# Kernel tuning notes

Hardware: AMD Instinct MI355X
Metric: run time of the kernel (lower is better)

Reference implementation:

```python
import jax, jax.numpy as jnp
import numpy as np

N_NODES = 10000
LN_EPS = 1e-5


def _gcn(x, W, b, src, dst):
    # GraphConvolution: linear transform then sum-aggregate messages over edges.
    sup = x @ W                               # [B, N, H]
    msg = sup[:, src, :]                      # [B, E, H] gather from source nodes
    agg = jax.vmap(lambda m: jax.ops.segment_sum(m, dst, num_segments=N_NODES))(msg)
    return agg + b


def _layernorm(x, g, b):
    mu = jnp.mean(x, axis=-1, keepdims=True)
    var = jnp.var(x, axis=-1, keepdims=True)
    return (x - mu) * jax.lax.rsqrt(var + LN_EPS) * g + b


def _attention_pool(x, W, u, num_iterations=3):
    # x: [B, N, d] -> r: [B, 1, d]
    a = jnp.tanh(x @ W) @ u                   # [B, N]
    alpha = jax.nn.softmax(a, axis=1)
    r = jnp.einsum('bn,bnd->bd', alpha, x)
    for _ in range(num_iterations):
        beta = jax.nn.softmax(jnp.einsum('bnd,bd->bn', x, r), axis=1)
        r = jnp.einsum('bn,bnd->bd', beta, x)
    return r[:, None, :]


def _forward(x, src, dst, W_conv0, b_conv0, W_convs, b_convs,
             mW1, mb1, mW2, mb2, mW3, mb3,
             ln1_g, ln1_b, ln2_g, ln2_b, attnW, attnu, fW1, fb1, fW2, fb2,
             fcW, fcb):
    gelu = lambda t: jax.nn.gelu(t, approximate=False)
    # stacked GCN layers (first layer distinct input dim)
    x = gelu(_gcn(x, W_conv0, b_conv0, src, dst))
    for i in range(W_convs.shape[0]):
        x = gelu(_gcn(x, W_convs[i], b_convs[i], src, dst))
    # dropout is identity in eval mode
    # MLP head
    x = jax.nn.relu(x @ mW1 + mb1)
    x = jax.nn.relu(x @ mW2 + mb2)
    x = x @ mW3 + mb3
    # Encoder: 2 layers of (attention-pool residual + LN + FFN residual + LN)
    for i in range(2):
        x = x + _attention_pool(x, attnW[i], attnu[i])   # broadcast [B,1,d]
        x = _layernorm(x, ln1_g[i], ln1_b[i])
        h = jax.nn.relu(x @ fW1[i] + fb1[i]) @ fW2[i] + fb2[i]
        x = _layernorm(x + h, ln2_g[i], ln2_b[i])
    x = x @ fcW + fcb                          # [B, N, out]
    return x.mean(axis=1)                      # [B, out]


def setup_inputs() -> dict:
    key = jax.random.key(0)
    ks = jax.random.split(key, 32)
    B, N, E = 4, N_NODES, 160000
    F_in, H, D, A, OUT = 128, 256, 256, 8, 10
    s = lambda k, *shape: jax.random.normal(k, shape, jnp.float32) * 0.05
    return {
        'x': jax.random.normal(ks[0], (B, N, F_in), jnp.float32),
        'src': jax.random.randint(ks[1], (E,), 0, N, jnp.int32),
        'dst': jax.random.randint(ks[2], (E,), 0, N, jnp.int32),
        'W_conv0': s(ks[3], F_in, H), 'b_conv0': s(ks[4], H),
        'W_convs': s(ks[5], 3, H, H), 'b_convs': s(ks[6], 3, H),
        'mW1': s(ks[7], H, H // 2), 'mb1': s(ks[8], H // 2),
        'mW2': s(ks[9], H // 2, H // 4), 'mb2': s(ks[10], H // 4),
        'mW3': s(ks[11], H // 4, D), 'mb3': s(ks[12], D),
        'ln1_g': jnp.ones((2, D), jnp.float32), 'ln1_b': jnp.zeros((2, D), jnp.float32),
        'ln2_g': jnp.ones((2, D), jnp.float32), 'ln2_b': jnp.zeros((2, D), jnp.float32),
        'attnW': s(ks[13], 2, D, A), 'attnu': s(ks[14], 2, A),
        'fW1': s(ks[15], 2, D, H), 'fb1': s(ks[16], 2, H),
        'fW2': s(ks[17], 2, H, D), 'fb2': s(ks[18], 2, D),
        'fcW': s(ks[19], D, OUT), 'fcb': s(ks[20], OUT),
    }


def reference(x, src, dst, W_conv0, b_conv0, W_convs, b_convs,
              mW1, mb1, mW2, mb2, mW3, mb3,
              ln1_g, ln1_b, ln2_g, ln2_b, attnW, attnu, fW1, fb1, fW2, fb2,
              fcW, fcb):
    return _forward(x, src, dst, W_conv0, b_conv0, W_convs, b_convs,
                    mW1, mb1, mW2, mb2, mW3, mb3,
                    ln1_g, ln1_b, ln2_g, ln2_b, attnW, attnu, fW1, fb1, fW2, fb2,
                    fcW, fcb)
```

## Files before the change

kernel.cpp:

```cpp
#include <hip/hip_runtime.h>
#include <math.h>

#define NN 10000
#define NB 4
#define NE 160000
#define DM 256
#define MR (NB * NN)
#define LN_EPS 1e-5f
#define PCH 40
#define NCH (NN / PCH)
#define CCH 100

typedef __attribute__((ext_vector_type(8))) short short8;
typedef __attribute__((ext_vector_type(4))) float floatx4;


__device__ inline float bf2f(unsigned short u) {
    unsigned int x = ((unsigned int)u) << 16;
    float f;
    __builtin_memcpy(&f, &x, 4);
    return f;
}

__device__ inline unsigned short f2bf(float f) {
    unsigned int x;
    __builtin_memcpy(&x, &f, 4);
    unsigned int r = x + 0x7FFFu + ((x >> 16) & 1u);
    return (unsigned short)(r >> 16);
}

__device__ inline float gelu_exact(float x) {
    return 0.5f * x * (1.0f + erff(x * 0.70710678118654752f));
}

__device__ inline float waveAllReduce(float v) {
#pragma unroll
    for (int off = 32; off > 0; off >>= 1) v += __shfl_xor(v, off, 64);
    return v;
}

__device__ inline void gld16(const unsigned short* g, unsigned short* l) {
    __builtin_amdgcn_global_load_lds((const __attribute__((address_space(1))) void*)g,
                                     (__attribute__((address_space(3))) void*)l, 16, 0, 0);
}


__global__ void zero_i32_kernel(int* p, int n) {
    int i = blockIdx.x * 256 + threadIdx.x;
    if (i < n) p[i] = 0;
}

__global__ void cvt_bf16_kernel(const float* __restrict__ in, unsigned short* __restrict__ out, int n) {
    int i = blockIdx.x * 256 + threadIdx.x;
    if (i < n) out[i] = f2bf(in[i]);
}

struct TD { const float* src; unsigned short* dst; int K; int N; };
struct TDs { TD d[11]; };

__global__ void transpose_all_kernel(TDs tds) {
    TD t = tds.d[blockIdx.y];
    int idx = blockIdx.x * 256 + threadIdx.x;
    int total = t.K * t.N;
    if (idx < total) {
        int n = idx / t.K;
        int k = idx - n * t.K;
        t.dst[idx] = f2bf(t.src[(size_t)k * t.N + n]);
    }
}


__global__ void hist_kernel(const int* __restrict__ dst, int* __restrict__ counts, int e) {
    int i = blockIdx.x * 256 + threadIdx.x;
    if (i < e) atomicAdd(&counts[dst[i]], 1);
}

__global__ __launch_bounds__(256) void scan_kernel(const int* __restrict__ counts,
                                                   int* __restrict__ row_ptr,
                                                   int* __restrict__ fill_pos, int n) {
    __shared__ int sums[256];
    int tid = threadIdx.x;
    int chunk = (n + 255) / 256;
    int s0 = tid * chunk;
    int s1 = min(n, s0 + chunk);
    int local = 0;
    for (int i = s0; i < s1; i++) local += counts[i];
    sums[tid] = local;
    __syncthreads();
    for (int off = 1; off < 256; off <<= 1) {
        int v = (tid >= off) ? sums[tid - off] : 0;
        __syncthreads();
        sums[tid] += v;
        __syncthreads();
    }
    int base = (tid == 0) ? 0 : sums[tid - 1];
    for (int i = s0; i < s1; i++) {
        row_ptr[i] = base;
        fill_pos[i] = base;
        base += counts[i];
    }
    if (tid == 255) row_ptr[n] = sums[255];
}

__global__ void fill_kernel(const int* __restrict__ src, const int* __restrict__ dst,
                            int* __restrict__ fill_pos, int* __restrict__ csr_src, int e) {
    int i = blockIdx.x * 256 + threadIdx.x;
    if (i < e) {
        int p = atomicAdd(&fill_pos[dst[i]], 1);
        csr_src[p] = src[i];
    }
}


template <int BN, int CM>
__global__ __launch_bounds__(256) void mfma_gemm_kernel(
    const unsigned short* __restrict__ A, const unsigned short* __restrict__ Bt,
    const float* __restrict__ bias, void* __restrict__ Cp, int K, int N, int act) {
    constexpr int NBF = BN / 32;
    __shared__ unsigned short AsL[4 * 64 * 8];
    __shared__ unsigned short BsL[(BN / 16) * 64 * 8];

    const int tid = threadIdx.x;
    const int w = tid >> 6, l = tid & 63;
    const int wm = w >> 1, wn = w & 1;
    const int bm0 = blockIdx.y * 64;
    const int bn0 = blockIdx.x * BN;
    const int lm = l & 15, lq = l >> 4;

    floatx4 acc[2][NBF];
#pragma unroll
    for (int mi = 0; mi < 2; mi++)
#pragma unroll
        for (int ni = 0; ni < NBF; ni++) acc[mi][ni] = (floatx4){0.f, 0.f, 0.f, 0.f};

    const int s_ll = tid & 63;
    const int a_row = bm0 + (tid >> 6) * 16 + (s_ll & 15);
    const int s_kc = (s_ll >> 4) * 8;

    for (int k0 = 0; k0 < K; k0 += 32) {
        gld16(&A[(size_t)a_row * K + k0 + s_kc], &AsL[tid * 8]);
#pragma unroll
        for (int cc = 0; cc < BN / 64; cc++) {
            int c = tid + cc * 256;
            int rown = bn0 + (c >> 6) * 16 + (c & 15);
            int kc = k0 + ((c & 63) >> 4) * 8;
            gld16(&Bt[(size_t)rown * K + kc], &BsL[c * 8]);
        }
        __syncthreads();
        short8 af[2], bfv[NBF];
#pragma unroll
        for (int mi = 0; mi < 2; mi++) af[mi] = *(short8*)&AsL[((wm * 2 + mi) * 64 + l) * 8];
#pragma unroll
        for (int ni = 0; ni < NBF; ni++) bfv[ni] = *(short8*)&BsL[((wn * NBF + ni) * 64 + l) * 8];
#pragma unroll
        for (int mi = 0; mi < 2; mi++)
#pragma unroll
            for (int ni = 0; ni < NBF; ni++)
                acc[mi][ni] = __builtin_amdgcn_mfma_f32_16x16x32_bf16(af[mi], bfv[ni], acc[mi][ni], 0, 0, 0);
        __syncthreads();
    }

#pragma unroll
    for (int ni = 0; ni < NBF; ni++) {
        int col = bn0 + (wn * NBF + ni) * 16 + lm;
        float bv = bias ? bias[col] : 0.0f;
#pragma unroll
        for (int mi = 0; mi < 2; mi++) {
            int row0 = bm0 + (wm * 2 + mi) * 16 + lq * 4;
#pragma unroll
            for (int r = 0; r < 4; r++) {
                int row = row0 + r;
                float v = acc[mi][ni][r] + bv;
                if (act == 1) v = fmaxf(v, 0.0f);
                if (CM == 0) {
                    ((float*)Cp)[(size_t)row * N + col] = v;
                } else if (CM == 1) {
                    ((unsigned short*)Cp)[(size_t)row * N + col] = f2bf(v);
                } else {
                    int bb = row / NN;
                    int nn = row - bb * NN;
                    ((unsigned short*)Cp)[(size_t)nn * (NB * DM) + bb * DM + col] = f2bf(v);
                }
            }
        }
    }
}


__global__ __launch_bounds__(256) void agg_kernel(const unsigned short* __restrict__ sup,
                                                  const int* __restrict__ row_ptr,
                                                  const int* __restrict__ csr_src,
                                                  const float* __restrict__ bias,
                                                  unsigned short* __restrict__ out) {
    int n = blockIdx.x;
    int w = threadIdx.x >> 6, l = threadIdx.x & 63;
    int s = row_ptr[n], e = row_ptr[n + 1];
    const int off = w * DM + l * 4;
    float a0 = 0.f, a1 = 0.f, a2 = 0.f, a3 = 0.f;
    int j = s;
    for (; j + 8 <= e; j += 8) {
        int idx[8];
#pragma unroll
        for (int k = 0; k < 8; k++) idx[k] = csr_src[j + k];
        ushort4 v[8];
#pragma unroll
        for (int k = 0; k < 8; k++) v[k] = *(const ushort4*)&sup[(size_t)idx[k] * (NB * DM) + off];
#pragma unroll
        for (int k = 0; k < 8; k++) {
            a0 += bf2f(v[k].x); a1 += bf2f(v[k].y);
            a2 += bf2f(v[k].z); a3 += bf2f(v[k].w);
        }
    }
    for (; j < e; j++) {
        ushort4 v = *(const ushort4*)&sup[(size_t)csr_src[j] * (NB * DM) + off];
        a0 += bf2f(v.x); a1 += bf2f(v.y); a2 += bf2f(v.z); a3 += bf2f(v.w);
    }
    int d0 = l * 4;
    const float4 bv = *(const float4*)&bias[d0];
    ushort4 o;
    o.x = f2bf(gelu_exact(a0 + bv.x));
    o.y = f2bf(gelu_exact(a1 + bv.y));
    o.z = f2bf(gelu_exact(a2 + bv.z));
    o.w = f2bf(gelu_exact(a3 + bv.w));
    *(ushort4*)&out[((size_t)w * NN + n) * DM + d0] = o;
}


template <int MODE>
__global__ __launch_bounds__(256) void attn_pool_kernel(const unsigned short* __restrict__ x16,
                                                        const float* __restrict__ W,
                                                        const float* __restrict__ u,
                                                        const float* __restrict__ r_in,
                                                        float* __restrict__ pm,
                                                        float* __restrict__ pl,
                                                        float* __restrict__ pv) {
    int c = blockIdx.x, b = blockIdx.y;
    int tid = threadIdx.x, w = tid >> 6, l = tid & 63;
    float4 rv = {0, 0, 0, 0};
    float u0[8];
    if (MODE == 1) {
        rv = *(const float4*)&r_in[b * DM + l * 4];
    } else {
#pragma unroll
        for (int j = 0; j < 8; j++) u0[j] = u[j];
    }
    int n0 = c * PCH;
    float m = -INFINITY, L = 0.0f;
    float v0 = 0.f, v1 = 0.f, v2 = 0.f, v3 = 0.f;
    for (int n = n0 + w; n < n0 + PCH; n += 4) {
        ushort4 xb = *(const ushort4*)&x16[((size_t)b * NN + n) * DM + l * 4];
        float x0 = bf2f(xb.x), x1 = bf2f(xb.y), x2 = bf2f(xb.z), x3 = bf2f(xb.w);
        float s;
        if (MODE == 1) {
            s = x0 * rv.x + x1 * rv.y + x2 * rv.z + x3 * rv.w;
            s = waveAllReduce(s);
        } else {
            const float4* Wv = (const float4*)W;
            int d0 = l * 4;
            float xs[4] = {x0, x1, x2, x3};
            float t[8] = {0, 0, 0, 0, 0, 0, 0, 0};
#pragma unroll
            for (int dd = 0; dd < 4; dd++) {
                float4 w0 = Wv[(d0 + dd) * 2 + 0];
                float4 w1 = Wv[(d0 + dd) * 2 + 1];
                t[0] += xs[dd] * w0.x; t[1] += xs[dd] * w0.y; t[2] += xs[dd] * w0.z; t[3] += xs[dd] * w0.w;
                t[4] += xs[dd] * w1.x; t[5] += xs[dd] * w1.y; t[6] += xs[dd] * w1.z; t[7] += xs[dd] * w1.w;
            }
#pragma unroll
            for (int jj = 0; jj < 8; jj++) t[jj] = waveAllReduce(t[jj]);
            s = 0.f;
#pragma unroll
            for (int jj = 0; jj < 8; jj++) s += tanhf(t[jj]) * u0[jj];
        }
        if (s > m) {
            float sc = __expf(m - s);
            L *= sc; v0 *= sc; v1 *= sc; v2 *= sc; v3 *= sc;
            m = s;
        }
        float wgt = __expf(s - m);
        L += wgt;
        v0 += wgt * x0; v1 += wgt * x1; v2 += wgt * x2; v3 += wgt * x3;
    }
    __shared__ float sm[4], sl[4];
    __shared__ float sv[4][DM];
    if (l == 0) { sm[w] = m; sl[w] = L; }
    float4 vv = {v0, v1, v2, v3};
    *(float4*)&sv[w][l * 4] = vv;
    __syncthreads();
    int d = tid;
    float M = fmaxf(fmaxf(sm[0], sm[1]), fmaxf(sm[2], sm[3]));
    float e0 = __expf(sm[0] - M), e1 = __expf(sm[1] - M);
    float e2 = __expf(sm[2] - M), e3 = __expf(sm[3] - M);
    float Lt = e0 * sl[0] + e1 * sl[1] + e2 * sl[2] + e3 * sl[3];
    float vd = e0 * sv[0][d] + e1 * sv[1][d] + e2 * sv[2][d] + e3 * sv[3][d];
    pv[((size_t)b * NCH + c) * DM + d] = vd;
    if (d == 0) {
        pm[b * NCH + c] = M;
        pl[b * NCH + c] = Lt;
    }
}

__global__ __launch_bounds__(256) void attn_combine_kernel(const float* __restrict__ pm,
                                                           const float* __restrict__ pl,
                                                           const float* __restrict__ pv,
                                                           float* __restrict__ r) {
    int b = blockIdx.x, tid = threadIdx.x;
    __shared__ float red[256];
    __shared__ float se[NCH];
    float mv = -INFINITY;
    for (int c = tid; c < NCH; c += 256) mv = fmaxf(mv, pm[b * NCH + c]);
    red[tid] = mv;
    __syncthreads();
    for (int off = 128; off > 0; off >>= 1) {
        if (tid < off) red[tid] = fmaxf(red[tid], red[tid + off]);
        __syncthreads();
    }
    float M = red[0];
    __syncthreads();
    float lsum = 0.0f;
    for (int c = tid; c < NCH; c += 256) {
        float e = __expf(pm[b * NCH + c] - M);
        se[c] = e;
        lsum += e * pl[b * NCH + c];
    }
    red[tid] = lsum;
    __syncthreads();
    for (int off = 128; off > 0; off >>= 1) {
        if (tid < off) red[tid] += red[tid + off];
        __syncthreads();
    }
    float L = red[0];
    __syncthreads();
    float acc = 0.0f;
    for (int c = 0; c < NCH; c++) acc += se[c] * pv[((size_t)b * NCH + c) * DM + tid];
    r[b * DM + tid] = acc / L;
}


__global__ __launch_bounds__(256) void ln_bcast_kernel(const unsigned short* __restrict__ x16,
                                                       const float* __restrict__ r,
                                                       const float* __restrict__ g,
                                                       const float* __restrict__ bt,
                                                       unsigned short* __restrict__ out16) {
    int l = threadIdx.x & 63, w = threadIdx.x >> 6;
    int row = blockIdx.x * 4 + w;
    int b = row / NN;
    ushort4 xb = *(const ushort4*)&x16[(size_t)row * DM + l * 4];
    float4 rv = *(const float4*)(r + (size_t)b * DM + l * 4);
    float4 y;
    y.x = bf2f(xb.x) + rv.x; y.y = bf2f(xb.y) + rv.y;
    y.z = bf2f(xb.z) + rv.z; y.w = bf2f(xb.w) + rv.w;
    float s = y.x + y.y + y.z + y.w;
    float sq = y.x * y.x + y.y * y.y + y.z * y.z + y.w * y.w;
    s = waveAllReduce(s);
    sq = waveAllReduce(sq);
    float mean = s * (1.0f / 256.0f);
    float var = sq * (1.0f / 256.0f) - mean * mean;
    float rstd = rsqrtf(var + LN_EPS);
    float4 gv = *(const float4*)(g + l * 4);
    float4 bv = *(const float4*)(bt + l * 4);
    ushort4 o;
    o.x = f2bf((y.x - mean) * rstd * gv.x + bv.x);
    o.y = f2bf((y.y - mean) * rstd * gv.y + bv.y);
    o.z = f2bf((y.z - mean) * rstd * gv.z + bv.z);
    o.w = f2bf((y.w - mean) * rstd * gv.w + bv.w);
    *(ushort4*)&out16[(size_t)row * DM + l * 4] = o;
}

__global__ __launch_bounds__(256) void ln_elem_kernel(const unsigned short* __restrict__ x16,
                                                      const float* __restrict__ h,
                                                      const float* __restrict__ g,
                                                      const float* __restrict__ bt,
                                                      unsigned short* __restrict__ out16) {
    int l = threadIdx.x & 63, w = threadIdx.x >> 6;
    int row = blockIdx.x * 4 + w;
    ushort4 xb = *(const ushort4*)&x16[(size_t)row * DM + l * 4];
    float4 hv = *(const float4*)(h + (size_t)row * DM + l * 4);
    float4 y;
    y.x = bf2f(xb.x) + hv.x; y.y = bf2f(xb.y) + hv.y;
    y.z = bf2f(xb.z) + hv.z; y.w = bf2f(xb.w) + hv.w;
    float s = y.x + y.y + y.z + y.w;
    float sq = y.x * y.x + y.y * y.y + y.z * y.z + y.w * y.w;
    s = waveAllReduce(s);
    sq = waveAllReduce(sq);
    float mean = s * (1.0f / 256.0f);
    float var = sq * (1.0f / 256.0f) - mean * mean;
    float rstd = rsqrtf(var + LN_EPS);
    float4 gv = *(const float4*)(g + l * 4);
    float4 bv = *(const float4*)(bt + l * 4);
    ushort4 o;
    o.x = f2bf((y.x - mean) * rstd * gv.x + bv.x);
    o.y = f2bf((y.y - mean) * rstd * gv.y + bv.y);
    o.z = f2bf((y.z - mean) * rstd * gv.z + bv.z);
    o.w = f2bf((y.w - mean) * rstd * gv.w + bv.w);
    *(ushort4*)&out16[(size_t)row * DM + l * 4] = o;
}


__global__ __launch_bounds__(256) void colsum_kernel(const unsigned short* __restrict__ x16,
                                                     float* __restrict__ pcol) {
    int b = blockIdx.y, c = blockIdx.x, d = threadIdx.x;
    int n0 = c * CCH, n1 = n0 + CCH;
    float acc = 0.0f;
    for (int n = n0; n < n1; n++) acc += bf2f(x16[((size_t)b * NN + n) * DM + d]);
    pcol[((size_t)b * (NN / CCH) + c) * DM + d] = acc;
}

__global__ __launch_bounds__(256) void final_kernel(const float* __restrict__ pcol,
                                                    const float* __restrict__ fcW,
                                                    const float* __restrict__ fcb,
                                                    float* __restrict__ out) {
    int b = blockIdx.x, d = threadIdx.x;
    __shared__ float sx[DM];
    float acc = 0.0f;
    for (int c = 0; c < NN / CCH; c++) acc += pcol[((size_t)b * (NN / CCH) + c) * DM + d];
    sx[d] = acc;
    __syncthreads();
    if (d < 10) {
        float o = 0.0f;
        for (int k = 0; k < DM; k++) o += sx[k] * fcW[k * 10 + d];
        out[b * 10 + d] = o * (1.0f / NN) + fcb[d];
    }
}


extern "C" void kernel_launch(void* const* d_in, const int* in_sizes, int n_in,
                              void* d_out, int out_size, void* d_ws, size_t ws_size,
                              hipStream_t stream) {
    const float* x_in    = (const float*)d_in[0];
    const int*   src     = (const int*)d_in[1];
    const int*   dst     = (const int*)d_in[2];
    const float* W_conv0 = (const float*)d_in[3];
    const float* b_conv0 = (const float*)d_in[4];
    const float* W_convs = (const float*)d_in[5];
    const float* b_convs = (const float*)d_in[6];
    const float* mW1 = (const float*)d_in[7];
    const float* mb1 = (const float*)d_in[8];
    const float* mW2 = (const float*)d_in[9];
    const float* mb2 = (const float*)d_in[10];
    const float* mW3 = (const float*)d_in[11];
    const float* mb3 = (const float*)d_in[12];
    const float* ln1_g = (const float*)d_in[13];
    const float* ln1_b = (const float*)d_in[14];
    const float* ln2_g = (const float*)d_in[15];
    const float* ln2_b = (const float*)d_in[16];
    const float* attnW = (const float*)d_in[17];
    const float* attnu = (const float*)d_in[18];
    const float* fW1 = (const float*)d_in[19];
    const float* fb1 = (const float*)d_in[20];
    const float* fW2 = (const float*)d_in[21];
    const float* fb2 = (const float*)d_in[22];
    const float* fcW = (const float*)d_in[23];
    const float* fcb = (const float*)d_in[24];
    float* out = (float*)d_out;

    char* p = (char*)d_ws;
    auto alloc = [&](size_t bytes) { char* q = p; p += (bytes + 255) & ~(size_t)255; return q; };
    float* A = (float*)alloc((size_t)MR * DM * 4);
    unsigned short* sup16 = (unsigned short*)alloc((size_t)MR * DM * 2);
    unsigned short* act16 = (unsigned short*)alloc((size_t)MR * DM * 2);
    unsigned short* b16   = (unsigned short*)alloc((size_t)MR * DM * 2);
    unsigned short* t1    = (unsigned short*)alloc((size_t)MR * 128 * 2);
    unsigned short* t2    = (unsigned short*)alloc((size_t)MR * 64 * 2);
    unsigned short* wt    = (unsigned short*)alloc((size_t)548864 * 2);
    float* rbuf = (float*)alloc(NB * DM * 4);
    float* pm0  = (float*)alloc(NB * NCH * 4);
    float* pl0  = (float*)alloc(NB * NCH * 4);
    float* pv0  = (float*)alloc((size_t)NB * NCH * DM * 4);
    float* pcol = (float*)alloc((size_t)NB * (NN / CCH) * DM * 4);
    int* counts   = (int*)alloc(NN * 4);
    int* row_ptr  = (int*)alloc((NN + 1) * 4);
    int* fill_pos = (int*)alloc(NN * 4);
    int* csr_src  = (int*)alloc(NE * 4);

    unsigned short* Wt_conv0 = wt;
    unsigned short* Wt_convs = Wt_conv0 + 32768;
    unsigned short* mW1t = Wt_convs + 196608;
    unsigned short* mW2t = mW1t + 32768;
    unsigned short* mW3t = mW2t + 8192;
    unsigned short* fW1t = mW3t + 16384;
    unsigned short* fW2t = fW1t + 131072;

    const dim3 blk(256);

    zero_i32_kernel<<<(NN + 255) / 256, blk, 0, stream>>>(counts, NN);
    hist_kernel<<<(NE + 255) / 256, blk, 0, stream>>>(dst, counts, NE);
    scan_kernel<<<1, blk, 0, stream>>>(counts, row_ptr, fill_pos, NN);
    fill_kernel<<<(NE + 255) / 256, blk, 0, stream>>>(src, dst, fill_pos, csr_src, NE);

    TDs tds;
    tds.d[0]  = {W_conv0, Wt_conv0, 128, 256};
    tds.d[1]  = {W_convs + 0 * 65536, Wt_convs + 0 * 65536, 256, 256};
    tds.d[2]  = {W_convs + 1 * 65536, Wt_convs + 1 * 65536, 256, 256};
    tds.d[3]  = {W_convs + 2 * 65536, Wt_convs + 2 * 65536, 256, 256};
    tds.d[4]  = {mW1, mW1t, 256, 128};
    tds.d[5]  = {mW2, mW2t, 128, 64};
    tds.d[6]  = {mW3, mW3t, 64, 256};
    tds.d[7]  = {fW1 + 0 * 65536, fW1t + 0 * 65536, 256, 256};
    tds.d[8]  = {fW1 + 1 * 65536, fW1t + 1 * 65536, 256, 256};
    tds.d[9]  = {fW2 + 0 * 65536, fW2t + 0 * 65536, 256, 256};
    tds.d[10] = {fW2 + 1 * 65536, fW2t + 1 * 65536, 256, 256};
    transpose_all_kernel<<<dim3(256, 11), blk, 0, stream>>>(tds);

    cvt_bf16_kernel<<<(MR * 128 + 255) / 256, blk, 0, stream>>>(x_in, t1, MR * 128);

    mfma_gemm_kernel<128, 2><<<dim3(2, MR / 64), blk, 0, stream>>>(t1, Wt_conv0, nullptr, sup16, 128, 256, 0);
    agg_kernel<<<NN, blk, 0, stream>>>(sup16, row_ptr, csr_src, b_conv0, act16);
    for (int i = 0; i < 3; i++) {
        mfma_gemm_kernel<128, 2><<<dim3(2, MR / 64), blk, 0, stream>>>(act16, Wt_convs + (size_t)i * 65536, nullptr, sup16, 256, 256, 0);
        agg_kernel<<<NN, blk, 0, stream>>>(sup16, row_ptr, csr_src, b_convs + (size_t)i * 256, act16);
    }

    mfma_gemm_kernel<128, 1><<<dim3(1, MR / 64), blk, 0, stream>>>(act16, mW1t, mb1, t1, 256, 128, 1);
    mfma_gemm_kernel<64, 1><<<dim3(1, MR / 64), blk, 0, stream>>>(t1, mW2t, mb2, t2, 128, 64, 1);
    mfma_gemm_kernel<128, 1><<<dim3(2, MR / 64), blk, 0, stream>>>(t2, mW3t, mb3, act16, 64, 256, 0);

    const dim3 poolGrid(NCH, NB);
    for (int i = 0; i < 2; i++) {
        const float* Wp = attnW + (size_t)i * DM * 8;
        const float* up = attnu + (size_t)i * 8;
        attn_pool_kernel<0><<<poolGrid, blk, 0, stream>>>(act16, Wp, up, nullptr, pm0, pl0, pv0);
        attn_combine_kernel<<<NB, blk, 0, stream>>>(pm0, pl0, pv0, rbuf);
        for (int it = 0; it < 3; it++) {
            attn_pool_kernel<1><<<poolGrid, blk, 0, stream>>>(act16, nullptr, nullptr, rbuf, pm0, pl0, pv0);
            attn_combine_kernel<<<NB, blk, 0, stream>>>(pm0, pl0, pv0, rbuf);
        }
        ln_bcast_kernel<<<MR / 4, blk, 0, stream>>>(act16, rbuf, ln1_g + (size_t)i * DM,
                                                    ln1_b + (size_t)i * DM, b16);
        mfma_gemm_kernel<128, 1><<<dim3(2, MR / 64), blk, 0, stream>>>(b16, fW1t + (size_t)i * 65536,
                                                                       fb1 + (size_t)i * DM, sup16, 256, 256, 1);
        mfma_gemm_kernel<128, 0><<<dim3(2, MR / 64), blk, 0, stream>>>(sup16, fW2t + (size_t)i * 65536,
                                                                       fb2 + (size_t)i * DM, A, 256, 256, 0);
        ln_elem_kernel<<<MR / 4, blk, 0, stream>>>(b16, A, ln2_g + (size_t)i * DM,
                                                   ln2_b + (size_t)i * DM, act16);
    }

    colsum_kernel<<<dim3(NN / CCH, NB), blk, 0, stream>>>(act16, pcol);
    final_kernel<<<NB, blk, 0, stream>>>(pcol, fcW, fcb, out);
}
```

Before: 790.9 us.

## Double-buffer MFMA GEMM loads and fuse FFN second GEMM with residual LayerNorm

Makes K a template parameter and double-buffers the LDS tiles, so the next K-slice is loaded while MFMAs run on the current one and one barrier per iteration goes away. Adds a gemm_ln_kernel that computes the full 256-wide FFN output row block, adds bias and residual, reduces row statistics across the two wave columns through shared memory, and writes the normalized bf16 output directly. This removes the fp32 intermediate buffer and the separate ln_elem pass, at the cost of a larger per-block tile, more registers and fewer blocks for that GEMM.

After: 770.8 us. 1.03x faster.

```diff
diff --git a/kernel.cpp b/kernel.cpp
--- a/kernel.cpp
+++ b/kernel.cpp
@@ -36,6 +36,12 @@
 __device__ inline float waveAllReduce(float v) {
 #pragma unroll
     for (int off = 32; off > 0; off >>= 1) v += __shfl_xor(v, off, 64);
+    return v;
+}
+
+__device__ inline float group16Reduce(float v) {
+#pragma unroll
+    for (int off = 8; off > 0; off >>= 1) v += __shfl_xor(v, off, 64);
     return v;
 }
 
@@ -112,13 +118,14 @@
 }
 
 
-template <int BN, int CM>
+template <int BN, int CM, int K>
 __global__ __launch_bounds__(256) void mfma_gemm_kernel(
     const unsigned short* __restrict__ A, const unsigned short* __restrict__ Bt,
-    const float* __restrict__ bias, void* __restrict__ Cp, int K, int N, int act) {
+    const float* __restrict__ bias, void* __restrict__ Cp, int N, int act) {
     constexpr int NBF = BN / 32;
-    __shared__ unsigned short AsL[4 * 64 * 8];
-    __shared__ unsigned short BsL[(BN / 16) * 64 * 8];
+    constexpr int NI = K / 32;
+    __shared__ unsigned short AsL[2][4 * 64 * 8];
+    __shared__ unsigned short BsL[2][(BN / 16) * 64 * 8];
 
     const int tid = threadIdx.x;
     const int w = tid >> 6, l = tid & 63;
@@ -133,31 +140,46 @@
 #pragma unroll
         for (int ni = 0; ni < NBF; ni++) acc[mi][ni] = (floatx4){0.f, 0.f, 0.f, 0.f};
 
-    const int s_ll = tid & 63;
-    const int a_row = bm0 + (tid >> 6) * 16 + (s_ll & 15);
-    const int s_kc = (s_ll >> 4) * 8;
-
-    for (int k0 = 0; k0 < K; k0 += 32) {
-        gld16(&A[(size_t)a_row * K + k0 + s_kc], &AsL[tid * 8]);
-#pragma unroll
-        for (int cc = 0; cc < BN / 64; cc++) {
-            int c = tid + cc * 256;
-            int rown = bn0 + (c >> 6) * 16 + (c & 15);
-            int kc = k0 + ((c & 63) >> 4) * 8;
-            gld16(&Bt[(size_t)rown * K + kc], &BsL[c * 8]);
-        }
+    const int a_row = bm0 + (tid >> 6) * 16 + (l & 15);
+    const int s_kc = (l >> 4) * 8;
+    int b_rown[BN / 64], b_kc[BN / 64];
+#pragma unroll
+    for (int cc = 0; cc < BN / 64; cc++) {
+        int c = tid + cc * 256;
+        b_rown[cc] = bn0 + (c >> 6) * 16 + (c & 15);
+        b_kc[cc] = ((c & 63) >> 4) * 8;
+    }
+
+    gld16(&A[(size_t)a_row * K + s_kc], &AsL[0][tid * 8]);
+#pragma unroll
+    for (int cc = 0; cc < BN / 64; cc++) {
+        int c = tid + cc * 256;
+        gld16(&Bt[(size_t)b_rown[cc] * K + b_kc[cc]], &BsL[0][c * 8]);
+    }
+
+#pragma unroll
+    for (int i = 0; i < NI; i++) {
+        const int buf = i & 1;
         __syncthreads();
+        if (i + 1 < NI) {
+            int k0 = (i + 1) * 32;
+            gld16(&A[(size_t)a_row * K + k0 + s_kc], &AsL[buf ^ 1][tid * 8]);
+#pragma unroll
+            for (int cc = 0; cc < BN / 64; cc++) {
+                int c = tid + cc * 256;
+                gld16(&Bt[(size_t)b_rown[cc] * K + k0 + b_kc[cc]], &BsL[buf ^ 1][c * 8]);
+            }
+        }
         short8 af[2], bfv[NBF];
 #pragma unroll
-        for (int mi = 0; mi < 2; mi++) af[mi] = *(short8*)&AsL[((wm * 2 + mi) * 64 + l) * 8];
-#pragma unroll
-        for (int ni = 0; ni < NBF; ni++) bfv[ni] = *(short8*)&BsL[((wn * NBF + ni) * 64 + l) * 8];
+        for (int mi = 0; mi < 2; mi++) af[mi] = *(short8*)&AsL[buf][((wm * 2 + mi) * 64 + l) * 8];
+#pragma unroll
+        for (int ni = 0; ni < NBF; ni++) bfv[ni] = *(short8*)&BsL[buf][((wn * NBF + ni) * 64 + l) * 8];
 #pragma unroll
         for (int mi = 0; mi < 2; mi++)
 #pragma unroll
             for (int ni = 0; ni < NBF; ni++)
                 acc[mi][ni] = __builtin_amdgcn_mfma_f32_16x16x32_bf16(af[mi], bfv[ni], acc[mi][ni], 0, 0, 0);
-        __syncthreads();
     }
 
 #pragma unroll
@@ -181,6 +203,136 @@
                     int nn = row - bb * NN;
                     ((unsigned short*)Cp)[(size_t)nn * (NB * DM) + bb * DM + col] = f2bf(v);
                 }
+            }
+        }
+    }
+}
+
+
+__global__ __launch_bounds__(256) void gemm_ln_kernel(
+    const unsigned short* __restrict__ A,
+    const unsigned short* __restrict__ Bt,
+    const float* __restrict__ bias,
+    const unsigned short* __restrict__ x1,
+    const float* __restrict__ g, const float* __restrict__ bt,
+    unsigned short* __restrict__ out16) {
+    constexpr int K = 256, NBF = 8, NI = K / 32;
+    __shared__ unsigned short AsL[2][4 * 64 * 8];
+    __shared__ unsigned short BsL[2][16 * 64 * 8];
+    __shared__ float rs[2][64], rq[2][64];
+
+    const int tid = threadIdx.x;
+    const int w = tid >> 6, l = tid & 63;
+    const int wm = w >> 1, wn = w & 1;
+    const int bm0 = blockIdx.x * 64;
+    const int lm = l & 15, lq = l >> 4;
+
+    floatx4 acc[2][NBF];
+#pragma unroll
+    for (int mi = 0; mi < 2; mi++)
+#pragma unroll
+        for (int ni = 0; ni < NBF; ni++) acc[mi][ni] = (floatx4){0.f, 0.f, 0.f, 0.f};
+
+    const int a_row = bm0 + (tid >> 6) * 16 + (l & 15);
+    const int s_kc = (l >> 4) * 8;
+    int b_rown[4], b_kc[4];
+#pragma unroll
+    for (int cc = 0; cc < 4; cc++) {
+        int c = tid + cc * 256;
+        b_rown[cc] = (c >> 6) * 16 + (c & 15);
+        b_kc[cc] = ((c & 63) >> 4) * 8;
+    }
+
+    gld16(&A[(size_t)a_row * K + s_kc], &AsL[0][tid * 8]);
+#pragma unroll
+    for (int cc = 0; cc < 4; cc++) {
+        int c = tid + cc * 256;
+        gld16(&Bt[(size_t)b_rown[cc] * K + b_kc[cc]], &BsL[0][c * 8]);
+    }
+
+#pragma unroll
+    for (int i = 0; i < NI; i++) {
+        const int buf = i & 1;
+        __syncthreads();
+        if (i + 1 < NI) {
+            int k0 = (i + 1) * 32;
+            gld16(&A[(size_t)a_row * K + k0 + s_kc], &AsL[buf ^ 1][tid * 8]);
+#pragma unroll
+            for (int cc = 0; cc < 4; cc++) {
+                int c = tid + cc * 256;
+                gld16(&Bt[(size_t)b_rown[cc] * K + k0 + b_kc[cc]], &BsL[buf ^ 1][c * 8]);
+            }
+        }
+        short8 af[2], bfv[NBF];
+#pragma unroll
+        for (int mi = 0; mi < 2; mi++) af[mi] = *(short8*)&AsL[buf][((wm * 2 + mi) * 64 + l) * 8];
+#pragma unroll
+        for (int ni = 0; ni < NBF; ni++) bfv[ni] = *(short8*)&BsL[buf][((wn * NBF + ni) * 64 + l) * 8];
+#pragma unroll
+        for (int mi = 0; mi < 2; mi++)
+#pragma unroll
+            for (int ni = 0; ni < NBF; ni++)
+                acc[mi][ni] = __builtin_amdgcn_mfma_f32_16x16x32_bf16(af[mi], bfv[ni], acc[mi][ni], 0, 0, 0);
+    }
+
+    float fb[NBF], gv[NBF], bv[NBF];
+#pragma unroll
+    for (int ni = 0; ni < NBF; ni++) {
+        int col = (wn * NBF + ni) * 16 + lm;
+        fb[ni] = bias[col];
+        gv[ni] = g[col];
+        bv[ni] = bt[col];
+    }
+    float psum[2][4], psq[2][4];
+#pragma unroll
+    for (int mi = 0; mi < 2; mi++)
+#pragma unroll
+        for (int r = 0; r < 4; r++) { psum[mi][r] = 0.f; psq[mi][r] = 0.f; }
+
+#pragma unroll
+    for (int mi = 0; mi < 2; mi++) {
+        int row0 = bm0 + (wm * 2 + mi) * 16 + lq * 4;
+#pragma unroll
+        for (int r = 0; r < 4; r++) {
+#pragma unroll
+            for (int ni = 0; ni < NBF; ni++) {
+                int col = (wn * NBF + ni) * 16 + lm;
+                float y = bf2f(x1[(size_t)(row0 + r) * DM + col]) + acc[mi][ni][r] + fb[ni];
+                acc[mi][ni][r] = y;
+                psum[mi][r] += y;
+                psq[mi][r] += y * y;
+            }
+        }
+    }
+#pragma unroll
+    for (int mi = 0; mi < 2; mi++)
+#pragma unroll
+        for (int r = 0; r < 4; r++) {
+            float s = group16Reduce(psum[mi][r]);
+            float q = group16Reduce(psq[mi][r]);
+            if (lm == 0) {
+                int rl = (wm * 2 + mi) * 16 + lq * 4 + r;
+                rs[wn][rl] = s;
+                rq[wn][rl] = q;
+            }
+        }
+    __syncthreads();
+#pragma unroll
+    for (int mi = 0; mi < 2; mi++) {
+        int row0 = bm0 + (wm * 2 + mi) * 16 + lq * 4;
+#pragma unroll
+        for (int r = 0; r < 4; r++) {
+            int rl = (wm * 2 + mi) * 16 + lq * 4 + r;
+            float s = rs[0][rl] + rs[1][rl];
+            float q = rq[0][rl] + rq[1][rl];
+            float mean = s * (1.0f / 256.0f);
+            float var = q * (1.0f / 256.0f) - mean * mean;
+            float rstd = rsqrtf(var + LN_EPS);
+#pragma unroll
+            for (int ni = 0; ni < NBF; ni++) {
+                int col = (wn * NBF + ni) * 16 + lm;
+                out16[(size_t)(row0 + r) * DM + col] =
+                    f2bf((acc[mi][ni][r] - mean) * rstd * gv[ni] + bv[ni]);
             }
         }
     }
@@ -350,35 +502,6 @@
     float4 y;
     y.x = bf2f(xb.x) + rv.x; y.y = bf2f(xb.y) + rv.y;
     y.z = bf2f(xb.z) + rv.z; y.w = bf2f(xb.w) + rv.w;
-    float s = y.x + y.y + y.z + y.w;
-    float sq = y.x * y.x + y.y * y.y + y.z * y.z + y.w * y.w;
-    s = waveAllReduce(s);
-    sq = waveAllReduce(sq);
-    float mean = s * (1.0f / 256.0f);
-    float var = sq * (1.0f / 256.0f) - mean * mean;
-    float rstd = rsqrtf(var + LN_EPS);
-    float4 gv = *(const float4*)(g + l * 4);
-    float4 bv = *(const float4*)(bt + l * 4);
-    ushort4 o;
-    o.x = f2bf((y.x - mean) * rstd * gv.x + bv.x);
-    o.y = f2bf((y.y - mean) * rstd * gv.y + bv.y);
-    o.z = f2bf((y.z - mean) * rstd * gv.z + bv.z);
-    o.w = f2bf((y.w - mean) * rstd * gv.w + bv.w);
-    *(ushort4*)&out16[(size_t)row * DM + l * 4] = o;
-}
-
-__global__ __launch_bounds__(256) void ln_elem_kernel(const unsigned short* __restrict__ x16,
-                                                      const float* __restrict__ h,
-                                                      const float* __restrict__ g,
-                                                      const float* __restrict__ bt,
-                                                      unsigned short* __restrict__ out16) {
-    int l = threadIdx.x & 63, w = threadIdx.x >> 6;
-    int row = blockIdx.x * 4 + w;
-    ushort4 xb = *(const ushort4*)&x16[(size_t)row * DM + l * 4];
-    float4 hv = *(const float4*)(h + (size_t)row * DM + l * 4);
-    float4 y;
-    y.x = bf2f(xb.x) + hv.x; y.y = bf2f(xb.y) + hv.y;
-    y.z = bf2f(xb.z) + hv.z; y.w = bf2f(xb.w) + hv.w;
     float s = y.x + y.y + y.z + y.w;
     float sq = y.x * y.x + y.y * y.y + y.z * y.z + y.w * y.w;
     s = waveAllReduce(s);
@@ -456,7 +579,6 @@
 
     char* p = (char*)d_ws;
     auto alloc = [&](size_t bytes) { char* q = p; p += (bytes + 255) & ~(size_t)255; return q; };
-    float* A = (float*)alloc((size_t)MR * DM * 4);
     unsigned short* sup16 = (unsigned short*)alloc((size_t)MR * DM * 2);
     unsigned short* act16 = (unsigned short*)alloc((size_t)MR * DM * 2);
     unsigned short* b16   = (unsigned short*)alloc((size_t)MR * DM * 2);
@@ -504,16 +626,16 @@
 
     cvt_bf16_kernel<<<(MR * 128 + 255) / 256, blk, 0, stream>>>(x_in, t1, MR * 128);
 
-    mfma_gemm_kernel<128, 2><<<dim3(2, MR / 64), blk, 0, stream>>>(t1, Wt_conv0, nullptr, sup16, 128, 256, 0);
+    mfma_gemm_kernel<128, 2, 128><<<dim3(2, MR / 64), blk, 0, stream>>>(t1, Wt_conv0, nullptr, sup16, 256, 0);
     agg_kernel<<<NN, blk, 0, stream>>>(sup16, row_ptr, csr_src, b_conv0, act16);
     for (int i = 0; i < 3; i++) {
-        mfma_gemm_kernel<128, 2><<<dim3(2, MR / 64), blk, 0, stream>>>(act16, Wt_convs + (size_t)i * 65536, nullptr, sup16, 256, 256, 0);
+        mfma_gemm_kernel<128, 2, 256><<<dim3(2, MR / 64), blk, 0, stream>>>(act16, Wt_convs + (size_t)i * 65536, nullptr, sup16, 256, 0);
         agg_kernel<<<NN, blk, 0, stream>>>(sup16, row_ptr, csr_src, b_convs + (size_t)i * 256, act16);
     }
 
-    mfma_gemm_kernel<128, 1><<<dim3(1, MR / 64), blk, 0, stream>>>(act16, mW1t, mb1, t1, 256, 128, 1);
-    mfma_gemm_kernel<64, 1><<<dim3(1, MR / 64), blk, 0, stream>>>(t1, mW2t, mb2, t2, 128, 64, 1);
-    mfma_gemm_kernel<128, 1><<<dim3(2, MR / 64), blk, 0, stream>>>(t2, mW3t, mb3, act16, 64, 256, 0);
+    mfma_gemm_kernel<128, 1, 256><<<dim3(1, MR / 64), blk, 0, stream>>>(act16, mW1t, mb1, t1, 128, 1);
+    mfma_gemm_kernel<64, 1, 128><<<dim3(1, MR / 64), blk, 0, stream>>>(t1, mW2t, mb2, t2, 64, 1);
+    mfma_gemm_kernel<128, 1, 64><<<dim3(2, MR / 64), blk, 0, stream>>>(t2, mW3t, mb3, act16, 256, 0);
 
     const dim3 poolGrid(NCH, NB);
     for (int i = 0; i < 2; i++) {
@@ -527,12 +649,12 @@
         }
         ln_bcast_kernel<<<MR / 4, blk, 0, stream>>>(act16, rbuf, ln1_g + (size_t)i * DM,
                                                     ln1_b + (size_t)i * DM, b16);
-        mfma_gemm_kernel<128, 1><<<dim3(2, MR / 64), blk, 0, stream>>>(b16, fW1t + (size_t)i * 65536,
-                                                                       fb1 + (size_t)i * DM, sup16, 256, 256, 1);
-        mfma_gemm_kernel<128, 0><<<dim3(2, MR / 64), blk, 0, stream>>>(sup16, fW2t + (size_t)i * 65536,
-                                                                       fb2 + (size_t)i * DM, A, 256, 256, 0);
-        ln_elem_kernel<<<MR / 4, blk, 0, stream>>>(b16, A, ln2_g + (size_t)i * DM,
-                                                   ln2_b + (size_t)i * DM, act16);
+        mfma_gemm_kernel<128, 1, 256><<<dim3(2, MR / 64), blk, 0, stream>>>(b16, fW1t + (size_t)i * 65536,
+                                                                            fb1 + (size_t)i * DM, sup16, 256, 1);
+        gemm_ln_kernel<<<MR / 64, blk, 0, stream>>>(sup16, fW2t + (size_t)i * 65536,
+                                                    fb2 + (size_t)i * DM, b16,
+                                                    ln2_g + (size_t)i * DM, ln2_b + (size_t)i * DM,
+                                                    act16);
     }
 
     colsum_kernel<<<dim3(NN / CCH, NB), blk, 0, stream>>>(act16, pcol);
```
